# Kernel tuning notes

Hardware: AMD Instinct MI355X
Metric: run time of the kernel (lower is better)

The kernel has to match this reference:

```python
import jax, jax.numpy as jnp
import numpy as np

N, D, H, F = 384, 512, 8, 64  # n_nodes, in/out features, heads, per-head hidden
SLOPE = 0.2


def gat_v2_layer(x, mask, W_l, W_r, a):
    """GATv2 layer (is_concat=True). x: [N, D_in]; mask: [N, N, 1] bool.

    torch semantics: g_sum[i, j] = g_l[j] + g_r[i]; e = a . LeakyReLU(g_sum);
    softmax over j (dim=1); aggregate g_r with einsum('ijh,jhf->ihf').
    attn linear nn.Linear(F, 1) is shared across heads -> a: [F].
    """
    n = x.shape[0]
    g_l = (x @ W_l).reshape(n, H, F)
    g_r = (x @ W_r).reshape(n, H, F)
    # pairwise [i, j, h, f] = g_r[i] + g_l[j]  (the big O(N^2) intermediate)
    s = jax.nn.leaky_relu(g_r[:, None] + g_l[None, :], negative_slope=SLOPE)
    e = jnp.einsum('ijhf,f->ijh', s, a)
    e = jnp.where(mask, e, -jnp.inf)
    att = jax.nn.softmax(e, axis=1)  # normalize over source nodes j
    out = jnp.einsum('ijh,jhf->ihf', att, g_r)
    return out.reshape(n, H * F)


def setup_inputs() -> dict:
    key = jax.random.key(0)
    ks = jax.random.split(key, 8)
    x = jax.random.normal(ks[0], (N, D), dtype=jnp.float32)
    adj = jax.random.randint(ks[1], (N, N, 1), 0, 2, dtype=jnp.int32)
    sd = 1.0 / np.sqrt(D)
    sa = 1.0 / np.sqrt(F)
    W_l0 = jax.random.normal(ks[2], (D, H * F), dtype=jnp.float32) * sd
    W_r0 = jax.random.normal(ks[3], (D, H * F), dtype=jnp.float32) * sd
    a0 = jax.random.normal(ks[4], (F,), dtype=jnp.float32) * sa
    W_l1 = jax.random.normal(ks[5], (H * F, H * F), dtype=jnp.float32) * sd
    W_r1 = jax.random.normal(ks[6], (H * F, H * F), dtype=jnp.float32) * sd
    a1 = jax.random.normal(ks[7], (F,), dtype=jnp.float32) * sa
    return {"x": x, "adj": adj, "W_l0": W_l0, "W_r0": W_r0, "a0": a0,
            "W_l1": W_l1, "W_r1": W_r1, "a1": a1}


def reference(x, adj, W_l0, W_r0, a0, W_l1, W_r1, a1):
    n = x.shape[0]
    # selfloop: fill diagonal of adj with 1
    idx = jnp.arange(n)
    adj = adj.at[idx, idx, 0].set(1)
    mask = adj != 0  # [N, N, 1]
    # layer 0: GATv2 -> ELU (i < n_layers-1) -> residual
    out = jax.nn.elu(gat_v2_layer(x, mask, W_l0, W_r0, a0))
    x = x + out
    # layer 1: GATv2 -> Identity -> residual
    out = gat_v2_layer(x, mask, W_l1, W_r1, a1)
    x = x + out
    return x
```

## Files before the change

kernel.cpp:

```cpp
#include <hip/hip_runtime.h>
#include <hip/hip_bf16.h>
#include <stdint.h>

typedef unsigned short ushort_t;
typedef unsigned long long u64;
typedef __attribute__((ext_vector_type(8))) short short8;
typedef __attribute__((ext_vector_type(4))) float f32x4;

#define N_NODES 384
#define HF      512
#define IT      12

__device__ inline ushort_t f2bf(float f) {
  __hip_bfloat16 b = __float2bfloat16(f);
  return *reinterpret_cast<ushort_t*>(&b);
}
__device__ inline float bf2f_u(ushort_t u) {
  union { float f; uint32_t i; } v; v.i = ((uint32_t)u) << 16; return v.f;
}
__device__ inline short8 pack8(const float* s) {
  short8 r;
#pragma unroll
  for (int j = 0; j < 8; ++j) r[j] = (short)f2bf(s[j]);
  return r;
}

__global__ __launch_bounds__(256) void gemm_direct(
    const float* __restrict__ X, const float* __restrict__ WL,
    const float* __restrict__ WR, float* __restrict__ G,
    ushort_t* __restrict__ glb, ushort_t* __restrict__ grT,
    const int* __restrict__ adj, u64* __restrict__ mbits)
{
  const int t = threadIdx.x, wave = t >> 6, lane = t & 63;
  const int lm = lane & 15, q = lane >> 4;
  const int m0 = blockIdx.x * 16;
  const int n0 = (blockIdx.y * 4 + wave) * 32;
  const float* Wp = (n0 < 512) ? (WL + n0) : (WR + (n0 - 512));
  const float* Arow = X + (m0 + lm) * HF;

  f32x4 acc0 = {0.f, 0.f, 0.f, 0.f};
  f32x4 acc1 = {0.f, 0.f, 0.f, 0.f};
#pragma unroll 4
  for (int kc = 0; kc < 16; ++kc) {
    const int kbase = kc * 32 + q * 8;
    float4 a0 = *(const float4*)(Arow + kbase);
    float4 a1 = *(const float4*)(Arow + kbase + 4);
    float av8[8] = {a0.x, a0.y, a0.z, a0.w, a1.x, a1.y, a1.z, a1.w};
    short8 af = pack8(av8);
    float b0f[8], b1f[8];
#pragma unroll
    for (int j = 0; j < 8; ++j) {
      const float* r = Wp + (kbase + j) * HF;
      b0f[j] = r[lm];
      b1f[j] = r[16 + lm];
    }
    short8 b0 = pack8(b0f);
    short8 b1 = pack8(b1f);
    acc0 = __builtin_amdgcn_mfma_f32_16x16x32_bf16(af, b0, acc0, 0, 0, 0);
    acc1 = __builtin_amdgcn_mfma_f32_16x16x32_bf16(af, b1, acc1, 0, 0, 0);
  }
  if (n0 < 512) {
#pragma unroll
    for (int r = 0; r < 4; ++r) {
      int m = m0 + q * 4 + r;
      glb[m * HF + n0 + lm]      = f2bf(acc0[r]);
      glb[m * HF + n0 + 16 + lm] = f2bf(acc1[r]);
    }
  } else {
#pragma unroll
    for (int r = 0; r < 4; ++r) {
      int m = m0 + q * 4 + r;
      G[m * 1024 + n0 + lm]      = acc0[r];
      G[m * 1024 + n0 + 16 + lm] = acc1[r];
    }
    int c0 = n0 - 512;
    uint2 p0, p1;
    p0.x = (uint32_t)f2bf(acc0[0]) | ((uint32_t)f2bf(acc0[1]) << 16);
    p0.y = (uint32_t)f2bf(acc0[2]) | ((uint32_t)f2bf(acc0[3]) << 16);
    p1.x = (uint32_t)f2bf(acc1[0]) | ((uint32_t)f2bf(acc1[1]) << 16);
    p1.y = (uint32_t)f2bf(acc1[2]) | ((uint32_t)f2bf(acc1[3]) << 16);
    *(uint2*)&grT[(c0 + lm) * 384 + m0 + q * 4]      = p0;
    *(uint2*)&grT[(c0 + 16 + lm) * 384 + m0 + q * 4] = p1;
  }
  if (adj != nullptr && blockIdx.y == 0) {
    int rbase = (blockIdx.x * 4 + wave) * 4;
    for (int rr = 0; rr < 4; ++rr) {
      int row = rbase + rr;
#pragma unroll
      for (int w = 0; w < 6; ++w) {
        int j = w * 64 + lane;
        u64 m = __ballot(adj[row * N_NODES + j] != 0 || row == j);
        if (lane == 0) mbits[row * 6 + w] = m;
      }
    }
  }
}

template <int LAYER>
__global__ __launch_bounds__(384) void attn_fused(
    const float* __restrict__ G, const ushort_t* __restrict__ glb,
    const ushort_t* __restrict__ grT, const u64* __restrict__ mbits,
    const float* __restrict__ resid_in, const float* __restrict__ avec,
    float* __restrict__ xcur_out, float* __restrict__ f_out)
{
  __shared__ __align__(16) char smem[49152];
  __shared__ float    s_e[IT][N_NODES];
  __shared__ ushort_t s_pb[16][392];
  __shared__ float s_bri[IT];
  __shared__ u64   s_mask[IT][6];
  ushort_t (*s_gl)[64] = (ushort_t(*)[64])smem;

  const int t = threadIdx.x;
  const int i0 = blockIdx.x * IT, h = blockIdx.y;
  const int lane = t & 63, wave = t >> 6;
  const int lm = lane & 15, q = lane >> 4;

#pragma unroll
  for (int rep = 0; rep < 8; ++rep) {
    int idx = rep * 384 + t, row = idx >> 3, cl = idx & 7;
    int cg = cl ^ (row & 7);
    const ushort_t* gsrc = glb + row * HF + h * 64 + cg * 8;
    __builtin_amdgcn_global_load_lds(
        (const __attribute__((address_space(1))) uint32_t*)gsrc,
        (__attribute__((address_space(3))) uint32_t*)(smem + idx * 16),
        16, 0, 0);
  }

  short8 bfrag[12];
  float  rres[4];
  if (wave < 4) {
    const ushort_t* Brow = grT + (h * 64 + wave * 16 + lm) * 384;
#pragma unroll
    for (int kc = 0; kc < 12; ++kc)
      bfrag[kc] = *(const short8*)&Brow[kc * 32 + q * 8];
    if (q < 3) {
#pragma unroll
      for (int r = 0; r < 4; ++r)
        rres[r] = resid_in[(i0 + q * 4 + r) * HF + h * 64 + wave * 16 + lm];
    }
  }

  if (t < 72) ((u64*)s_mask)[t] = mbits[i0 * 6 + t];
  if (t >= 128 && t < 320) {
    int u = t - 128, il = u >> 4, fg = u & 15;
    float4 g4 = *(const float4*)(G + (i0 + il) * 1024 + 512 + h * 64 + fg * 4);
    float4 a4 = *(const float4*)(avec + fg * 4);
    float s = a4.x * g4.x + a4.y * g4.y + a4.z * g4.z + a4.w * g4.w;
    s += __shfl_xor(s, 1); s += __shfl_xor(s, 2);
    s += __shfl_xor(s, 4); s += __shfl_xor(s, 8);
    if (fg == 0) s_bri[il] = s;
  }
#pragma unroll
  for (int r4 = 0; r4 < 4; ++r4) s_pb[IT + r4][t] = 0;
  __syncthreads();

  float gl[64], av[64];
  {
    const int sw = t & 7;
#pragma unroll
    for (int cg = 0; cg < 8; ++cg) {
      short8 v = *(const short8*)&s_gl[t][(cg ^ sw) * 8];
#pragma unroll
      for (int u2 = 0; u2 < 8; ++u2)
        gl[cg * 8 + u2] = bf2f_u((ushort_t)v[u2]);
    }
#pragma unroll
    for (int c = 0; c < 16; ++c) {
      float4 a4 = ((const float4*)avec)[c];
      av[c * 4] = a4.x; av[c * 4 + 1] = a4.y;
      av[c * 4 + 2] = a4.z; av[c * 4 + 3] = a4.w;
    }
  }
  float accl = 0.f;
#pragma unroll
  for (int f = 0; f < 64; ++f) accl += av[f] * gl[f];

  const int jw = t >> 6, jb = t & 63;
#pragma unroll
  for (int il = 0; il < IT; ++il) {
    const float4* gr4 = (const float4*)(G + (i0 + il) * 1024 + 512 + h * 64);
    float acc = 0.f;
#pragma unroll
    for (int c = 0; c < 16; ++c) {
      float4 g4 = gr4[c];
      acc += av[c * 4]     * fabsf(gl[c * 4]     + g4.x);
      acc += av[c * 4 + 1] * fabsf(gl[c * 4 + 1] + g4.y);
      acc += av[c * 4 + 2] * fabsf(gl[c * 4 + 2] + g4.z);
      acc += av[c * 4 + 3] * fabsf(gl[c * 4 + 3] + g4.w);
    }
    bool m = (s_mask[il][jw] >> jb) & 1;
    float e = 0.6f * (accl + s_bri[il]) + 0.4f * acc;
    s_e[il][t] = m ? e : -1e30f;
  }
  __syncthreads();

#pragma unroll
  for (int rep = 0; rep < 2; ++rep) {
    int il = wave * 2 + rep;
    float v[6];
    float mx = -1e30f;
#pragma unroll
    for (int c = 0; c < 6; ++c) { v[c] = s_e[il][lane + 64 * c]; mx = fmaxf(mx, v[c]); }
#pragma unroll
    for (int off = 32; off; off >>= 1) mx = fmaxf(mx, __shfl_xor(mx, off));
    float sum = 0.f;
#pragma unroll
    for (int c = 0; c < 6; ++c) { v[c] = __expf(v[c] - mx); sum += v[c]; }
#pragma unroll
    for (int off = 32; off; off >>= 1) sum += __shfl_xor(sum, off);
    float inv = 1.0f / sum;
#pragma unroll
    for (int c = 0; c < 6; ++c) s_pb[il][lane + 64 * c] = f2bf(v[c] * inv);
  }
  __syncthreads();

  if (wave < 4) {
    f32x4 acc = {0.f, 0.f, 0.f, 0.f};
#pragma unroll
    for (int kc = 0; kc < 12; ++kc) {
      short8 af = *(const short8*)&s_pb[lm][kc * 32 + q * 8];
      acc = __builtin_amdgcn_mfma_f32_16x16x32_bf16(af, bfrag[kc], acc, 0, 0, 0);
    }
    if (q < 3) {
#pragma unroll
      for (int r = 0; r < 4; ++r) {
        int i = i0 + q * 4 + r;
        int off = i * HF + h * 64 + wave * 16 + lm;
        float o = acc[r];
        if (LAYER == 0) {
          float oe = (o > 0.f) ? o : (__expf(o) - 1.f);
          xcur_out[off] = rres[r] + oe;
        } else {
          f_out[off] = rres[r] + o;
        }
      }
    }
  }
}

extern "C" void kernel_launch(void* const* d_in, const int* in_sizes, int n_in,
                              void* d_out, int out_size, void* d_ws, size_t ws_size,
                              hipStream_t stream) {
  const float* x   = (const float*)d_in[0];
  const int*   adj = (const int*)d_in[1];
  const float* Wl0 = (const float*)d_in[2];
  const float* Wr0 = (const float*)d_in[3];
  const float* a0  = (const float*)d_in[4];
  const float* Wl1 = (const float*)d_in[5];
  const float* Wr1 = (const float*)d_in[6];
  const float* a1  = (const float*)d_in[7];
  float* out = (float*)d_out;

  char* ws = (char*)d_ws;
  float*    G    = (float*)   (ws + 0L);
  ushort_t* grT  = (ushort_t*)(ws + (2L << 20));
  ushort_t* glb  = (ushort_t*)(ws + (3L << 20));
  u64*      mbits= (u64*)     (ws + (4L << 20));
  float*    xcur = (float*)   (ws + (5L << 20));

  gemm_direct<<<dim3(24, 8), 256, 0, stream>>>(x, Wl0, Wr0, G, glb, grT,
                                               adj, mbits);
  attn_fused<0><<<dim3(32, 8), 384, 0, stream>>>(G, glb, grT, mbits, x, a0,
                                                 xcur, nullptr);
  gemm_direct<<<dim3(24, 8), 256, 0, stream>>>(xcur, Wl1, Wr1, G, glb, grT,
                                               nullptr, nullptr);
  attn_fused<1><<<dim3(32, 8), 384, 0, stream>>>(G, glb, grT, mbits, xcur, a1,
                                                 nullptr, out);
}
```

Measured before the change: 119.5 us.

## Prepack weights and activations to bf16 K-major layout before GEMMs

A new prepack kernel converts both layers' weight matrices into a bf16 transposed (N-major, K-contiguous) layout and converts the input x to bf16. The GEMM then loads contiguous short8 fragments instead of doing strided fp32 gathers and per-element conversion. Layer 0's attention epilogue also writes a bf16 copy of its output so the layer-1 GEMM can read it directly. The cost is an extra kernel launch plus extra global traffic for the packed copies, which is repeated on every call.

```diff
diff --git a/kernel.cpp b/kernel.cpp
--- a/kernel.cpp
+++ b/kernel.cpp
@@ -25,9 +25,38 @@
   return r;
 }
 
+__global__ __launch_bounds__(256) void prepack(
+    const float* __restrict__ X,
+    const float* __restrict__ Wl0, const float* __restrict__ Wr0,
+    const float* __restrict__ Wl1, const float* __restrict__ Wr1,
+    ushort_t* __restrict__ Xbf, ushort_t* __restrict__ Wp0,
+    ushort_t* __restrict__ Wp1)
+{
+  const int bid = blockIdx.x, t = threadIdx.x;
+  if (bid < 512) {
+    int gid = bid * 256 + t;
+    int l   = gid >> 16;
+    int r   = gid & 65535;
+    int n   = r & 1023, kc = r >> 10;
+    const float* Wsrc = (n < 512) ? (l ? Wl1 : Wl0) : (l ? Wr1 : Wr0);
+    const int nn = n & 511;
+    float v[8];
+#pragma unroll
+    for (int j = 0; j < 8; ++j) v[j] = Wsrc[(kc * 8 + j) * 512 + nn];
+    ushort_t* dst = (l ? Wp1 : Wp0) + n * 512 + kc * 8;
+    *(short8*)dst = pack8(v);
+  } else {
+    int gid = (bid - 512) * 256 + t;
+    const float* src = X + gid * 8;
+    float4 a0 = *(const float4*)src, a1 = *(const float4*)(src + 4);
+    float v[8] = {a0.x, a0.y, a0.z, a0.w, a1.x, a1.y, a1.z, a1.w};
+    *(short8*)(Xbf + gid * 8) = pack8(v);
+  }
+}
+
 __global__ __launch_bounds__(256) void gemm_direct(
-    const float* __restrict__ X, const float* __restrict__ WL,
-    const float* __restrict__ WR, float* __restrict__ G,
+    const ushort_t* __restrict__ Xbf, const ushort_t* __restrict__ Wp,
+    float* __restrict__ G,
     ushort_t* __restrict__ glb, ushort_t* __restrict__ grT,
     const int* __restrict__ adj, u64* __restrict__ mbits)
 {
@@ -35,27 +64,18 @@
   const int lm = lane & 15, q = lane >> 4;
   const int m0 = blockIdx.x * 16;
   const int n0 = (blockIdx.y * 4 + wave) * 32;
-  const float* Wp = (n0 < 512) ? (WL + n0) : (WR + (n0 - 512));
-  const float* Arow = X + (m0 + lm) * HF;
+  const ushort_t* Arow  = Xbf + (m0 + lm) * 512;
+  const ushort_t* Brow0 = Wp + (n0 + lm) * 512;
+  const ushort_t* Brow1 = Wp + (n0 + 16 + lm) * 512;
 
   f32x4 acc0 = {0.f, 0.f, 0.f, 0.f};
   f32x4 acc1 = {0.f, 0.f, 0.f, 0.f};
-#pragma unroll 4
+#pragma unroll
   for (int kc = 0; kc < 16; ++kc) {
     const int kbase = kc * 32 + q * 8;
-    float4 a0 = *(const float4*)(Arow + kbase);
-    float4 a1 = *(const float4*)(Arow + kbase + 4);
-    float av8[8] = {a0.x, a0.y, a0.z, a0.w, a1.x, a1.y, a1.z, a1.w};
-    short8 af = pack8(av8);
-    float b0f[8], b1f[8];
-#pragma unroll
-    for (int j = 0; j < 8; ++j) {
-      const float* r = Wp + (kbase + j) * HF;
-      b0f[j] = r[lm];
-      b1f[j] = r[16 + lm];
-    }
-    short8 b0 = pack8(b0f);
-    short8 b1 = pack8(b1f);
+    short8 af = *(const short8*)(Arow + kbase);
+    short8 b0 = *(const short8*)(Brow0 + kbase);
+    short8 b1 = *(const short8*)(Brow1 + kbase);
     acc0 = __builtin_amdgcn_mfma_f32_16x16x32_bf16(af, b0, acc0, 0, 0, 0);
     acc1 = __builtin_amdgcn_mfma_f32_16x16x32_bf16(af, b1, acc1, 0, 0, 0);
   }
@@ -101,7 +121,8 @@
     const float* __restrict__ G, const ushort_t* __restrict__ glb,
     const ushort_t* __restrict__ grT, const u64* __restrict__ mbits,
     const float* __restrict__ resid_in, const float* __restrict__ avec,
-    float* __restrict__ xcur_out, float* __restrict__ f_out)
+    float* __restrict__ xcur_out, ushort_t* __restrict__ xbf_out,
+    float* __restrict__ f_out)
 {
   __shared__ __align__(16) char smem[49152];
   __shared__ float    s_e[IT][N_NODES];
@@ -229,7 +250,9 @@
         float o = acc[r];
         if (LAYER == 0) {
           float oe = (o > 0.f) ? o : (__expf(o) - 1.f);
-          xcur_out[off] = rres[r] + oe;
+          float v = rres[r] + oe;
+          xcur_out[off] = v;
+          xbf_out[off]  = f2bf(v);
         } else {
           f_out[off] = rres[r] + o;
         }
@@ -257,13 +280,18 @@
   ushort_t* glb  = (ushort_t*)(ws + (3L << 20));
   u64*      mbits= (u64*)     (ws + (4L << 20));
   float*    xcur = (float*)   (ws + (5L << 20));
-
-  gemm_direct<<<dim3(24, 8), 256, 0, stream>>>(x, Wl0, Wr0, G, glb, grT,
+  ushort_t* Xbf0 = (ushort_t*)(ws + (6L << 20));
+  ushort_t* xbfc = (ushort_t*)(ws + (7L << 20));
+  ushort_t* Wp0  = (ushort_t*)(ws + (8L << 20));
+  ushort_t* Wp1  = (ushort_t*)(ws + (9L << 20));
+
+  prepack<<<608, 256, 0, stream>>>(x, Wl0, Wr0, Wl1, Wr1, Xbf0, Wp0, Wp1);
+  gemm_direct<<<dim3(24, 8), 256, 0, stream>>>(Xbf0, Wp0, G, glb, grT,
                                                adj, mbits);
   attn_fused<0><<<dim3(32, 8), 384, 0, stream>>>(G, glb, grT, mbits, x, a0,
-                                                 xcur, nullptr);
-  gemm_direct<<<dim3(24, 8), 256, 0, stream>>>(xcur, Wl1, Wr1, G, glb, grT,
+                                                 xcur, xbfc, nullptr);
+  gemm_direct<<<dim3(24, 8), 256, 0, stream>>>(xbfc, Wp1, G, glb, grT,
                                                nullptr, nullptr);
   attn_fused<1><<<dim3(32, 8), 384, 0, stream>>>(G, glb, grT, mbits, xcur, a1,
-                                                 nullptr, out);
-}
+                                                 nullptr, nullptr, out);
+}
```

Result: no change. 121.0 us (+1.2%).

## Fuse all four launches into one cooperative kernel with grid syncs

Applied to the files above, without the earlier changes.

Replaces the two GEMM and two attention launches with a single cooperative kernel of 256 blocks that runs each phase in turn, separated by grid-wide barriers. The GEMM phase is retiled to one 16x16 output tile per wave so it maps onto the 256x6-wave grid, and the mask build is spread over blocks. The attention dot product is split into four independent accumulators to shorten the dependency chain. This removes launch gaps between kernels in exchange for grid-sync cost and a GEMM with half the per-wave work and less reuse of the A fragment.

```diff
diff --git a/kernel.cpp b/kernel.cpp
--- a/kernel.cpp
+++ b/kernel.cpp
@@ -1,6 +1,9 @@
 #include <hip/hip_runtime.h>
+#include <hip/hip_cooperative_groups.h>
 #include <hip/hip_bf16.h>
 #include <stdint.h>
+
+namespace cg = cooperative_groups;
 
 typedef unsigned short ushort_t;
 typedef unsigned long long u64;
@@ -25,7 +28,15 @@
   return r;
 }
 
-__global__ __launch_bounds__(256) void gemm_direct(
+struct SMem {
+  __align__(16) char gl_raw[49152];
+  float    e[IT][N_NODES];
+  ushort_t pb[16][392];
+  float    bri[IT];
+  u64      mask[IT][6];
+};
+
+__device__ __forceinline__ void gemm_phase(
     const float* __restrict__ X, const float* __restrict__ WL,
     const float* __restrict__ WR, float* __restrict__ G,
     ushort_t* __restrict__ glb, ushort_t* __restrict__ grT,
@@ -33,13 +44,13 @@
 {
   const int t = threadIdx.x, wave = t >> 6, lane = t & 63;
   const int lm = lane & 15, q = lane >> 4;
-  const int m0 = blockIdx.x * 16;
-  const int n0 = (blockIdx.y * 4 + wave) * 32;
+  const int tile = blockIdx.x * 6 + wave;
+  const int m0 = (tile >> 6) * 16;
+  const int n0 = (tile & 63) * 16;
   const float* Wp = (n0 < 512) ? (WL + n0) : (WR + (n0 - 512));
   const float* Arow = X + (m0 + lm) * HF;
 
-  f32x4 acc0 = {0.f, 0.f, 0.f, 0.f};
-  f32x4 acc1 = {0.f, 0.f, 0.f, 0.f};
+  f32x4 acc = {0.f, 0.f, 0.f, 0.f};
 #pragma unroll 4
   for (int kc = 0; kc < 16; ++kc) {
     const int kbase = kc * 32 + q * 8;
@@ -47,71 +58,51 @@
     float4 a1 = *(const float4*)(Arow + kbase + 4);
     float av8[8] = {a0.x, a0.y, a0.z, a0.w, a1.x, a1.y, a1.z, a1.w};
     short8 af = pack8(av8);
-    float b0f[8], b1f[8];
-#pragma unroll
-    for (int j = 0; j < 8; ++j) {
-      const float* r = Wp + (kbase + j) * HF;
-      b0f[j] = r[lm];
-      b1f[j] = r[16 + lm];
-    }
-    short8 b0 = pack8(b0f);
-    short8 b1 = pack8(b1f);
-    acc0 = __builtin_amdgcn_mfma_f32_16x16x32_bf16(af, b0, acc0, 0, 0, 0);
-    acc1 = __builtin_amdgcn_mfma_f32_16x16x32_bf16(af, b1, acc1, 0, 0, 0);
+    float bf[8];
+#pragma unroll
+    for (int j = 0; j < 8; ++j) bf[j] = Wp[(kbase + j) * HF + lm];
+    short8 b = pack8(bf);
+    acc = __builtin_amdgcn_mfma_f32_16x16x32_bf16(af, b, acc, 0, 0, 0);
   }
   if (n0 < 512) {
 #pragma unroll
     for (int r = 0; r < 4; ++r) {
       int m = m0 + q * 4 + r;
-      glb[m * HF + n0 + lm]      = f2bf(acc0[r]);
-      glb[m * HF + n0 + 16 + lm] = f2bf(acc1[r]);
+      glb[m * HF + n0 + lm] = f2bf(acc[r]);
     }
   } else {
 #pragma unroll
     for (int r = 0; r < 4; ++r) {
       int m = m0 + q * 4 + r;
-      G[m * 1024 + n0 + lm]      = acc0[r];
-      G[m * 1024 + n0 + 16 + lm] = acc1[r];
+      G[m * 1024 + n0 + lm] = acc[r];
     }
     int c0 = n0 - 512;
-    uint2 p0, p1;
-    p0.x = (uint32_t)f2bf(acc0[0]) | ((uint32_t)f2bf(acc0[1]) << 16);
-    p0.y = (uint32_t)f2bf(acc0[2]) | ((uint32_t)f2bf(acc0[3]) << 16);
-    p1.x = (uint32_t)f2bf(acc1[0]) | ((uint32_t)f2bf(acc1[1]) << 16);
-    p1.y = (uint32_t)f2bf(acc1[2]) | ((uint32_t)f2bf(acc1[3]) << 16);
-    *(uint2*)&grT[(c0 + lm) * 384 + m0 + q * 4]      = p0;
-    *(uint2*)&grT[(c0 + 16 + lm) * 384 + m0 + q * 4] = p1;
-  }
-  if (adj != nullptr && blockIdx.y == 0) {
-    int rbase = (blockIdx.x * 4 + wave) * 4;
-    for (int rr = 0; rr < 4; ++rr) {
-      int row = rbase + rr;
-#pragma unroll
-      for (int w = 0; w < 6; ++w) {
-        int j = w * 64 + lane;
-        u64 m = __ballot(adj[row * N_NODES + j] != 0 || row == j);
-        if (lane == 0) mbits[row * 6 + w] = m;
-      }
+    uint2 p;
+    p.x = (uint32_t)f2bf(acc[0]) | ((uint32_t)f2bf(acc[1]) << 16);
+    p.y = (uint32_t)f2bf(acc[2]) | ((uint32_t)f2bf(acc[3]) << 16);
+    *(uint2*)&grT[(c0 + lm) * 384 + m0 + q * 4] = p;
+  }
+  if (adj != nullptr && blockIdx.x < 64) {
+    int row = blockIdx.x * 6 + wave;
+#pragma unroll
+    for (int w = 0; w < 6; ++w) {
+      int j = w * 64 + lane;
+      u64 m = __ballot(adj[row * N_NODES + j] != 0 || row == j);
+      if (lane == 0) mbits[row * 6 + w] = m;
     }
   }
 }
 
 template <int LAYER>
-__global__ __launch_bounds__(384) void attn_fused(
-    const float* __restrict__ G, const ushort_t* __restrict__ glb,
+__device__ __forceinline__ void attn_phase(
+    SMem& sm, const float* __restrict__ G, const ushort_t* __restrict__ glb,
     const ushort_t* __restrict__ grT, const u64* __restrict__ mbits,
     const float* __restrict__ resid_in, const float* __restrict__ avec,
     float* __restrict__ xcur_out, float* __restrict__ f_out)
 {
-  __shared__ __align__(16) char smem[49152];
-  __shared__ float    s_e[IT][N_NODES];
-  __shared__ ushort_t s_pb[16][392];
-  __shared__ float s_bri[IT];
-  __shared__ u64   s_mask[IT][6];
-  ushort_t (*s_gl)[64] = (ushort_t(*)[64])smem;
-
+  ushort_t (*s_gl)[64] = (ushort_t(*)[64])sm.gl_raw;
   const int t = threadIdx.x;
-  const int i0 = blockIdx.x * IT, h = blockIdx.y;
+  const int i0 = (blockIdx.x & 31) * IT, h = blockIdx.x >> 5;
   const int lane = t & 63, wave = t >> 6;
   const int lm = lane & 15, q = lane >> 4;
 
@@ -122,7 +113,7 @@
     const ushort_t* gsrc = glb + row * HF + h * 64 + cg * 8;
     __builtin_amdgcn_global_load_lds(
         (const __attribute__((address_space(1))) uint32_t*)gsrc,
-        (__attribute__((address_space(3))) uint32_t*)(smem + idx * 16),
+        (__attribute__((address_space(3))) uint32_t*)(sm.gl_raw + idx * 16),
         16, 0, 0);
   }
 
@@ -140,7 +131,7 @@
     }
   }
 
-  if (t < 72) ((u64*)s_mask)[t] = mbits[i0 * 6 + t];
+  if (t < 72) ((u64*)sm.mask)[t] = mbits[i0 * 6 + t];
   if (t >= 128 && t < 320) {
     int u = t - 128, il = u >> 4, fg = u & 15;
     float4 g4 = *(const float4*)(G + (i0 + il) * 1024 + 512 + h * 64 + fg * 4);
@@ -148,10 +139,10 @@
     float s = a4.x * g4.x + a4.y * g4.y + a4.z * g4.z + a4.w * g4.w;
     s += __shfl_xor(s, 1); s += __shfl_xor(s, 2);
     s += __shfl_xor(s, 4); s += __shfl_xor(s, 8);
-    if (fg == 0) s_bri[il] = s;
-  }
-#pragma unroll
-  for (int r4 = 0; r4 < 4; ++r4) s_pb[IT + r4][t] = 0;
+    if (fg == 0) sm.bri[il] = s;
+  }
+#pragma unroll
+  for (int r4 = 0; r4 < 4; ++r4) sm.pb[IT + r4][t] = 0;
   __syncthreads();
 
   float gl[64], av[64];
@@ -179,18 +170,19 @@
 #pragma unroll
   for (int il = 0; il < IT; ++il) {
     const float4* gr4 = (const float4*)(G + (i0 + il) * 1024 + 512 + h * 64);
-    float acc = 0.f;
+    float c0 = 0.f, c1 = 0.f, c2 = 0.f, c3 = 0.f;
 #pragma unroll
     for (int c = 0; c < 16; ++c) {
       float4 g4 = gr4[c];
-      acc += av[c * 4]     * fabsf(gl[c * 4]     + g4.x);
-      acc += av[c * 4 + 1] * fabsf(gl[c * 4 + 1] + g4.y);
-      acc += av[c * 4 + 2] * fabsf(gl[c * 4 + 2] + g4.z);
-      acc += av[c * 4 + 3] * fabsf(gl[c * 4 + 3] + g4.w);
-    }
-    bool m = (s_mask[il][jw] >> jb) & 1;
-    float e = 0.6f * (accl + s_bri[il]) + 0.4f * acc;
-    s_e[il][t] = m ? e : -1e30f;
+      c0 += av[c * 4]     * fabsf(gl[c * 4]     + g4.x);
+      c1 += av[c * 4 + 1] * fabsf(gl[c * 4 + 1] + g4.y);
+      c2 += av[c * 4 + 2] * fabsf(gl[c * 4 + 2] + g4.z);
+      c3 += av[c * 4 + 3] * fabsf(gl[c * 4 + 3] + g4.w);
+    }
+    float acc = (c0 + c1) + (c2 + c3);
+    bool m = (sm.mask[il][jw] >> jb) & 1;
+    float e = 0.6f * (accl + sm.bri[il]) + 0.4f * acc;
+    sm.e[il][t] = m ? e : -1e30f;
   }
   __syncthreads();
 
@@ -200,7 +192,7 @@
     float v[6];
     float mx = -1e30f;
 #pragma unroll
-    for (int c = 0; c < 6; ++c) { v[c] = s_e[il][lane + 64 * c]; mx = fmaxf(mx, v[c]); }
+    for (int c = 0; c < 6; ++c) { v[c] = sm.e[il][lane + 64 * c]; mx = fmaxf(mx, v[c]); }
 #pragma unroll
     for (int off = 32; off; off >>= 1) mx = fmaxf(mx, __shfl_xor(mx, off));
     float sum = 0.f;
@@ -210,7 +202,7 @@
     for (int off = 32; off; off >>= 1) sum += __shfl_xor(sum, off);
     float inv = 1.0f / sum;
 #pragma unroll
-    for (int c = 0; c < 6; ++c) s_pb[il][lane + 64 * c] = f2bf(v[c] * inv);
+    for (int c = 0; c < 6; ++c) sm.pb[il][lane + 64 * c] = f2bf(v[c] * inv);
   }
   __syncthreads();
 
@@ -218,7 +210,7 @@
     f32x4 acc = {0.f, 0.f, 0.f, 0.f};
 #pragma unroll
     for (int kc = 0; kc < 12; ++kc) {
-      short8 af = *(const short8*)&s_pb[lm][kc * 32 + q * 8];
+      short8 af = *(const short8*)&sm.pb[lm][kc * 32 + q * 8];
       acc = __builtin_amdgcn_mfma_f32_16x16x32_bf16(af, bfrag[kc], acc, 0, 0, 0);
     }
     if (q < 3) {
@@ -236,6 +228,27 @@
       }
     }
   }
+}
+
+__global__ __launch_bounds__(384) void gat_fused(
+    const float* __restrict__ x, const int* __restrict__ adj,
+    const float* __restrict__ Wl0, const float* __restrict__ Wr0,
+    const float* __restrict__ a0, const float* __restrict__ Wl1,
+    const float* __restrict__ Wr1, const float* __restrict__ a1,
+    float* __restrict__ G, ushort_t* __restrict__ glb,
+    ushort_t* __restrict__ grT, u64* __restrict__ mbits,
+    float* __restrict__ xcur, float* __restrict__ out)
+{
+  __shared__ SMem sm;
+  cg::grid_group grid = cg::this_grid();
+
+  gemm_phase(x, Wl0, Wr0, G, glb, grT, adj, mbits);
+  grid.sync();
+  attn_phase<0>(sm, G, glb, grT, mbits, x, a0, xcur, nullptr);
+  grid.sync();
+  gemm_phase(xcur, Wl1, Wr1, G, glb, grT, nullptr, nullptr);
+  grid.sync();
+  attn_phase<1>(sm, G, glb, grT, mbits, xcur, a1, nullptr, out);
 }
 
 extern "C" void kernel_launch(void* const* d_in, const int* in_sizes, int n_in,
@@ -258,12 +271,8 @@
   u64*      mbits= (u64*)     (ws + (4L << 20));
   float*    xcur = (float*)   (ws + (5L << 20));
 
-  gemm_direct<<<dim3(24, 8), 256, 0, stream>>>(x, Wl0, Wr0, G, glb, grT,
-                                               adj, mbits);
-  attn_fused<0><<<dim3(32, 8), 384, 0, stream>>>(G, glb, grT, mbits, x, a0,
-                                                 xcur, nullptr);
-  gemm_direct<<<dim3(24, 8), 256, 0, stream>>>(xcur, Wl1, Wr1, G, glb, grT,
-                                               nullptr, nullptr);
-  attn_fused<1><<<dim3(32, 8), 384, 0, stream>>>(G, glb, grT, mbits, xcur, a1,
-                                                 nullptr, out);
-}
+  void* args[] = {&x, &adj, &Wl0, &Wr0, &a0, &Wl1, &Wr1, &a1,
+                  &G, &glb, &grT, &mbits, &xcur, &out};
+  hipLaunchCooperativeKernel((void*)gat_fused, dim3(256), dim3(384), args,
+                             0, stream);
+}
```

After: 230.0 us. +92.5%, slower.

## Stage weight tiles in LDS with double buffering; cache g_r rows in shared memory

Applied to the files above, without the earlier changes.

The projection GEMM now copies 64x128 fp32 weight tiles into double-buffered, swizzled LDS using async global_load_lds, instead of each lane issuing strided scalar global loads per k. In the attention kernel, the g_r rows for the block are kept in shared memory during setup, so the pairwise score loop reads LDS rather than global memory. The score accumulation is split into four independent partial sums to shorten the dependency chain. Costs are 64KB of LDS per GEMM block, which may reduce occupancy, plus an added barrier per k-chunk.

```diff
diff --git a/kernel.cpp b/kernel.cpp
--- a/kernel.cpp
+++ b/kernel.cpp
@@ -31,34 +31,65 @@
     ushort_t* __restrict__ glb, ushort_t* __restrict__ grT,
     const int* __restrict__ adj, u64* __restrict__ mbits)
 {
+  __shared__ __align__(16) float wtile[2][64 * 128];
+
   const int t = threadIdx.x, wave = t >> 6, lane = t & 63;
   const int lm = lane & 15, q = lane >> 4;
   const int m0 = blockIdx.x * 16;
   const int n0 = (blockIdx.y * 4 + wave) * 32;
-  const float* Wp = (n0 < 512) ? (WL + n0) : (WR + (n0 - 512));
+  const float* Wsrc = (blockIdx.y < 4) ? (WL + blockIdx.y * 128)
+                                       : (WR + (blockIdx.y - 4) * 128);
   const float* Arow = X + (m0 + lm) * HF;
+
+  const int colf0 = (((wave * 8) + (lm >> 2)) ^ ((q & 1) << 2)) * 4 + (lm & 3);
+  const int colf1 = (((wave * 8) + 4 + (lm >> 2)) ^ ((q & 1) << 2)) * 4 + (lm & 3);
+
+  auto stage = [&](int c) {
+    const float* base = Wsrc + c * 64 * HF;
+    char* dst0 = (char*)&wtile[c & 1][0];
+#pragma unroll
+    for (int rep = 0; rep < 8; ++rep) {
+      int idx = rep * 256 + t;
+      int k = idx >> 5, gp = idx & 31;
+      int gs = gp ^ (((k >> 3) & 1) << 2);
+      const float* src = base + k * HF + gs * 4;
+      __builtin_amdgcn_global_load_lds(
+          (const __attribute__((address_space(1))) uint32_t*)src,
+          (__attribute__((address_space(3))) uint32_t*)(dst0 + idx * 16),
+          16, 0, 0);
+    }
+  };
 
   f32x4 acc0 = {0.f, 0.f, 0.f, 0.f};
   f32x4 acc1 = {0.f, 0.f, 0.f, 0.f};
-#pragma unroll 4
-  for (int kc = 0; kc < 16; ++kc) {
-    const int kbase = kc * 32 + q * 8;
-    float4 a0 = *(const float4*)(Arow + kbase);
-    float4 a1 = *(const float4*)(Arow + kbase + 4);
-    float av8[8] = {a0.x, a0.y, a0.z, a0.w, a1.x, a1.y, a1.z, a1.w};
-    short8 af = pack8(av8);
-    float b0f[8], b1f[8];
-#pragma unroll
-    for (int j = 0; j < 8; ++j) {
-      const float* r = Wp + (kbase + j) * HF;
-      b0f[j] = r[lm];
-      b1f[j] = r[16 + lm];
-    }
-    short8 b0 = pack8(b0f);
-    short8 b1 = pack8(b1f);
-    acc0 = __builtin_amdgcn_mfma_f32_16x16x32_bf16(af, b0, acc0, 0, 0, 0);
-    acc1 = __builtin_amdgcn_mfma_f32_16x16x32_bf16(af, b1, acc1, 0, 0, 0);
-  }
+
+  stage(0);
+  for (int c = 0; c < 8; ++c) {
+    __syncthreads();
+    if (c < 7) stage(c + 1);
+    const float* buf = &wtile[c & 1][0];
+#pragma unroll
+    for (int i = 0; i < 2; ++i) {
+      const int kg = c * 64 + i * 32 + q * 8;
+      const int kl = i * 32 + q * 8;
+      float4 a0 = *(const float4*)(Arow + kg);
+      float4 a1 = *(const float4*)(Arow + kg + 4);
+      float av8[8] = {a0.x, a0.y, a0.z, a0.w, a1.x, a1.y, a1.z, a1.w};
+      short8 af = pack8(av8);
+      float b0f[8], b1f[8];
+#pragma unroll
+      for (int j = 0; j < 8; ++j) {
+        const float* r = buf + (kl + j) * 128;
+        b0f[j] = r[colf0];
+        b1f[j] = r[colf1];
+      }
+      short8 b0 = pack8(b0f);
+      short8 b1 = pack8(b1f);
+      acc0 = __builtin_amdgcn_mfma_f32_16x16x32_bf16(af, b0, acc0, 0, 0, 0);
+      acc1 = __builtin_amdgcn_mfma_f32_16x16x32_bf16(af, b1, acc1, 0, 0, 0);
+    }
+  }
+
   if (n0 < 512) {
 #pragma unroll
     for (int r = 0; r < 4; ++r) {
@@ -106,6 +137,7 @@
   __shared__ __align__(16) char smem[49152];
   __shared__ float    s_e[IT][N_NODES];
   __shared__ ushort_t s_pb[16][392];
+  __shared__ float    s_gr[IT][64];
   __shared__ float s_bri[IT];
   __shared__ u64   s_mask[IT][6];
   ushort_t (*s_gl)[64] = (ushort_t(*)[64])smem;
@@ -145,6 +177,7 @@
     int u = t - 128, il = u >> 4, fg = u & 15;
     float4 g4 = *(const float4*)(G + (i0 + il) * 1024 + 512 + h * 64 + fg * 4);
     float4 a4 = *(const float4*)(avec + fg * 4);
+    *(float4*)&s_gr[il][fg * 4] = g4;
     float s = a4.x * g4.x + a4.y * g4.y + a4.z * g4.z + a4.w * g4.w;
     s += __shfl_xor(s, 1); s += __shfl_xor(s, 2);
     s += __shfl_xor(s, 4); s += __shfl_xor(s, 8);
@@ -178,16 +211,16 @@
   const int jw = t >> 6, jb = t & 63;
 #pragma unroll
   for (int il = 0; il < IT; ++il) {
-    const float4* gr4 = (const float4*)(G + (i0 + il) * 1024 + 512 + h * 64);
-    float acc = 0.f;
+    float c0 = 0.f, c1 = 0.f, c2 = 0.f, c3 = 0.f;
 #pragma unroll
     for (int c = 0; c < 16; ++c) {
-      float4 g4 = gr4[c];
-      acc += av[c * 4]     * fabsf(gl[c * 4]     + g4.x);
-      acc += av[c * 4 + 1] * fabsf(gl[c * 4 + 1] + g4.y);
-      acc += av[c * 4 + 2] * fabsf(gl[c * 4 + 2] + g4.z);
-      acc += av[c * 4 + 3] * fabsf(gl[c * 4 + 3] + g4.w);
-    }
+      float4 g4 = *(const float4*)&s_gr[il][c * 4];
+      c0 += av[c * 4]     * fabsf(gl[c * 4]     + g4.x);
+      c1 += av[c * 4 + 1] * fabsf(gl[c * 4 + 1] + g4.y);
+      c2 += av[c * 4 + 2] * fabsf(gl[c * 4 + 2] + g4.z);
+      c3 += av[c * 4 + 3] * fabsf(gl[c * 4 + 3] + g4.w);
+    }
+    float acc = (c0 + c1) + (c2 + c3);
     bool m = (s_mask[il][jw] >> jb) & 1;
     float e = 0.6f * (accl + s_bri[il]) + 0.4f * acc;
     s_e[il][t] = m ? e : -1e30f;
```

Result: slower. 124.2 us (+3.9%).
